# Kernel tuning notes

Hardware: AMD Instinct MI355X
Metric: run time of the kernel (lower is better)

The kernel has to match this reference:

```python
import jax, jax.numpy as jnp
import numpy as np

B, S, V = 2, 336, 8      # batch, seq_len, n_vars
D, H, P = 256, 8, 96     # d_model, num_heads, pred_len
DK = D // H
OUT_CHN = 8
EPS = 1e-5


def _layernorm(x, g, b):
    mu = jnp.mean(x, axis=-1, keepdims=True)
    var = jnp.var(x, axis=-1, keepdims=True)
    return (x - mu) * jax.lax.rsqrt(var + EPS) * g + b


def _attn_ff(src, Wq, bq, Wk, bk, Wv, bv, Wo, bo, ln1_g, ln1_b):
    # src: [N, L, D]; manual MHA + residual + layernorm (dropout=0)
    N, L, _ = src.shape
    q = (src @ Wq + bq).reshape(N, L, H, DK).transpose(0, 2, 1, 3)
    k = (src @ Wk + bk).reshape(N, L, H, DK).transpose(0, 2, 1, 3)
    v = (src @ Wv + bv).reshape(N, L, H, DK).transpose(0, 2, 1, 3)
    scores = jnp.einsum('nhqd,nhkd->nhqk', q, k) / np.sqrt(DK).astype(np.float32)
    attn = jax.nn.softmax(scores, axis=-1)
    o = jnp.einsum('nhqk,nhkd->nhqd', attn, v)
    o = o.transpose(0, 2, 1, 3).reshape(N, L, D) @ Wo + bo
    return _layernorm(src + o, ln1_g, ln1_b)


def setup_inputs() -> dict:
    key = jax.random.key(0)
    ks = jax.random.split(key, 8)
    s = 1.0 / np.sqrt(D)
    return {
        'x': jax.random.normal(ks[0], (B, S, V), dtype=jnp.float32),
        'emb_w': jax.random.normal(ks[1], (1, D), dtype=jnp.float32),
        'emb_b': jnp.zeros((D,), jnp.float32),
        'Wq': jax.random.normal(ks[2], (D, D), dtype=jnp.float32) * s,
        'bq': jnp.zeros((D,), jnp.float32),
        'Wk': jax.random.normal(ks[3], (D, D), dtype=jnp.float32) * s,
        'bk': jnp.zeros((D,), jnp.float32),
        'Wv': jax.random.normal(ks[4], (D, D), dtype=jnp.float32) * s,
        'bv': jnp.zeros((D,), jnp.float32),
        'Wo': jax.random.normal(ks[5], (D, D), dtype=jnp.float32) * s,
        'bo': jnp.zeros((D,), jnp.float32),
        'ln1_g': jnp.ones((D,), jnp.float32),
        'ln1_b': jnp.zeros((D,), jnp.float32),
        'norm_g': jnp.ones((D,), jnp.float32),
        'norm_b': jnp.zeros((D,), jnp.float32),
        'proj_w': jax.random.normal(ks[6], (S * D, P), dtype=jnp.float32) / np.sqrt(S * D).astype(np.float32),
        'proj_b': jnp.zeros((P,), jnp.float32),
    }


def reference(x, emb_w, emb_b, Wq, bq, Wk, bk, Wv, bv, Wo, bo,
              ln1_g, ln1_b, norm_g, norm_b, proj_w, proj_b):
    attn_p = (Wq, bq, Wk, bk, Wv, bv, Wo, bo, ln1_g, ln1_b)
    # x: [B,S,V] -> [B,V,S] -> embed each scalar to D
    e = x.transpose(0, 2, 1)[..., None] @ emb_w + emb_b  # [B,V,S,D]
    for _ in range(10):
        # attention over time axis (shared weights)
        e = _attn_ff(e.reshape(B * V, S, D), *attn_p).reshape(B, V, S, D)
        e = _layernorm(e.transpose(0, 2, 1, 3), norm_g, norm_b)  # [B,S,V,D]
        # attention over variable axis (same weights)
        e = _attn_ff(e.reshape(B * S, V, D), *attn_p).reshape(B, S, V, D)
        e = e.transpose(0, 2, 1, 3)  # [B,V,S,D]
    out = e.reshape(B, V, S * D) @ proj_w + proj_b  # [B,V,P]
    return out.transpose(0, 2, 1)[:, :, :OUT_CHN]  # [B,P,out_chn]
```

## Files before the change

### kernel.cpp

```cpp
#include <hip/hip_runtime.h>

#define SS 336
#define VV 8
#define DD 256
#define DKK 32
#define NTOK 5376
#define NTD (NTOK * DD)
#define ATT_SCALE 0.17677669529663687f
#define LN_EPS 1e-5f

typedef _Float16 f16x8 __attribute__((ext_vector_type(8)));
typedef _Float16 f16x4v __attribute__((ext_vector_type(4)));
typedef __attribute__((ext_vector_type(4))) float f32x4;

__device__ inline _Float16 f2h(float f) { return (_Float16)f; }

__global__ __launch_bounds__(256) void k_init(
    const float* __restrict__ Wq, const float* __restrict__ Wk,
    const float* __restrict__ Wv, const float* __restrict__ Wo,
    const float* __restrict__ x, const float* __restrict__ ew,
    const float* __restrict__ eb, const float* __restrict__ PB,
    const float* __restrict__ PW,
    _Float16* __restrict__ WT2, float* __restrict__ E,
    _Float16* __restrict__ E16, _Float16* __restrict__ PWF,
    float* __restrict__ out) {
  int bid = blockIdx.x;
  int tid = threadIdx.x;
  if (bid < 1024) {
    int z = bid >> 8;
    const float* W = (z == 0) ? Wq : (z == 1) ? Wk : (z == 2) ? Wv : Wo;
    int o = (bid & 255) * 256 + tid;
    int blk = o >> 9;
    int idx = o & 511;
    int lane = idx >> 3, j = idx & 7;
    int nt = blk >> 3, kb = blk & 7;
    int lcol = lane & 15, quad = lane >> 4;
    int n = nt * 16 + lcol;
    int k = kb * 32 + quad * 8 + j;
    WT2[(size_t)z * 65536 + o] = f2h(W[k * 256 + n]);
    if (bid == 0) {
      for (int i = tid; i < 1536; i += 256) {
        int row = i / 96, p = i - row * 96;
        out[(row >> 3) * 768 + p * 8 + (row & 7)] = PB[p];
      }
    }
  } else if (bid < 6400) {
    int token = bid - 1024;
    int n = token / SS, s = token - n * SS;
    int b = n >> 3, v = n & 7;
    float xv = x[(b * SS + s) * VV + v];
    int d = tid;
    float val = fmaf(xv, ew[d], eb[d]);
    E[token * DD + d] = val;
    E16[token * DD + d] = f2h(val);
  } else {
    int idx = (bid - 6400) * 256 + tid;
    int ktile = idx / 384;
    int rem = idx - ktile * 384;
    int nt = rem >> 6, lane = rem & 63;
    int quad = lane >> 4, lcol = lane & 15;
    int k0 = ktile * 32 + quad * 8;
    int n = nt * 16 + lcol;
    f16x8 w;
#pragma unroll
    for (int j = 0; j < 8; ++j) w[j] = f2h(PW[(size_t)(k0 + j) * 96 + n]);
    *(f16x8*)&PWF[(size_t)idx * 8] = w;
  }
}

#define KSTR 36
#define VTSTR 344
#define PSTR 72
#define QSTR 40
__global__ __launch_bounds__(512) void k_attn_time(
    const _Float16* __restrict__ Et16, const _Float16* __restrict__ Q16,
    const _Float16* __restrict__ K16, const _Float16* __restrict__ V16,
    const _Float16* __restrict__ WT2,
    const float* __restrict__ bq, const float* __restrict__ bk,
    const float* __restrict__ bv, _Float16* __restrict__ O16, int mode) {
  int qg = blockIdx.x, h = blockIdx.y, n = blockIdx.z;
  int tid = threadIdx.x;
  int wave = tid >> 6, lane = tid & 63;
  int quad = lane >> 4, lcol = lane & 15;

  __shared__ __align__(16) char SMRAW[143264];
  _Float16* Ks  = (_Float16*)SMRAW;
  _Float16* Vt  = (_Float16*)(SMRAW + 24192);
  _Float16* Qs  = (_Float16*)(SMRAW + 46240);
  _Float16* Wl  = (_Float16*)(SMRAW + 60320);
  _Float16* Ach = (_Float16*)(SMRAW + 109472);
  _Float16* PsB = (_Float16*)(mode ? SMRAW + 60320 : SMRAW + 46240);

  const size_t ebase = (size_t)(n * SS) * DD;
  const size_t base  = ebase + h * DKK;
  int qt0 = qg ? 11 : 0;
  int qtend = qg ? 21 : 11;

  const f32x4 z4 = {0.f, 0.f, 0.f, 0.f};

  if (mode) {
    {
      int h2 = h * 2;
      for (int c = tid; c < 3072; c += 512) {
        int ot = c >> 9, rest = c & 511;
        int z = (ot < 2) ? 1 : (ot < 4) ? 2 : 0;
        int nt = h2 + (ot & 1);
        *(f16x8*)&Wl[(ot << 12) + rest * 8] =
            *(const f16x8*)&WT2[(size_t)z * 65536 + nt * 4096 + rest * 8];
      }
      for (int c = tid; c < 272; c += 512) {
        if (c < 256) {
          int d = c >> 3, col = 336 + (c & 7);
          Vt[d * VTSTR + col] = (_Float16)0.f;
        } else {
          Vt[32 * VTSTR + (c - 256)] = (_Float16)0.f;
        }
      }
    }
    for (int ck = 0; ck < 6; ++ck) {
      int m0c = ck * 64;
      int nmt = (ck < 5) ? 4 : 1;
      __syncthreads();
      for (int c = tid; c < nmt * 16 * 32; c += 512) {
        int row = c >> 5, seg = c & 31;
        *(f16x8*)&Ach[row * 264 + seg * 8] =
            *(const f16x8*)&Et16[ebase + (size_t)(m0c + row) * 256 + seg * 8];
      }
      __syncthreads();
      int nU = nmt * 6;
      for (int u = wave; u < nU; u += 8) {
        int mtl = u / 6, ot = u % 6;
        int gt = ck * 4 + mtl;
        if (ot >= 4 && (gt < qt0 || gt >= qtend)) continue;
        f32x4 acc = z4;
#pragma unroll
        for (int kb = 0; kb < 8; ++kb) {
          f16x8 af = *(const f16x8*)&Ach[(mtl * 16 + lcol) * 264 + kb * 32 + quad * 8];
          f16x8 wf = *(const f16x8*)&Wl[(ot << 12) + kb * 512 + lane * 8];
          acc = __builtin_amdgcn_mfma_f32_16x16x32_f16(af, wf, acc, 0, 0, 0);
        }
        int dlo = ((ot & 1) << 4) + lcol;
        const float* bz = (ot < 2) ? bk : (ot < 4) ? bv : bq;
        float bval = bz[h * 32 + dlo];
        if (ot < 2) {
#pragma unroll
          for (int i = 0; i < 4; ++i)
            Ks[(m0c + mtl * 16 + quad * 4 + i) * KSTR + dlo] = f2h(acc[i] + bval);
        } else if (ot < 4) {
#pragma unroll
          for (int i = 0; i < 4; ++i)
            Vt[dlo * VTSTR + (m0c + mtl * 16 + quad * 4 + i)] = f2h(acc[i] + bval);
        } else {
          int ql = gt - qt0;
#pragma unroll
          for (int i = 0; i < 4; ++i)
            Qs[(ql * 16 + quad * 4 + i) * QSTR + dlo] = f2h(acc[i] + bval);
        }
      }
    }
    __syncthreads();
  } else {
    for (int c = tid; c < 1344; c += 512) {
      int row = c >> 2, part = c & 3;
      f16x8 kv = *(const f16x8*)&K16[base + (size_t)row * DD + part * 8];
      f16x4v klo = __builtin_shufflevector(kv, kv, 0, 1, 2, 3);
      f16x4v khi = __builtin_shufflevector(kv, kv, 4, 5, 6, 7);
      *(f16x4v*)&Ks[row * KSTR + part * 8] = klo;
      *(f16x4v*)&Ks[row * KSTR + part * 8 + 4] = khi;
      f16x8 vv = *(const f16x8*)&V16[base + (size_t)row * DD + part * 8];
#pragma unroll
      for (int j = 0; j < 8; ++j) Vt[(part * 8 + j) * VTSTR + row] = vv[j];
    }
    for (int c = tid; c < 272; c += 512) {
      if (c < 256) {
        int d = c >> 3, col = 336 + (c & 7);
        Vt[d * VTSTR + col] = (_Float16)0.f;
      } else {
        Vt[32 * VTSTR + (c - 256)] = (_Float16)0.f;
      }
    }
    __syncthreads();
  }

  _Float16* P = PsB + wave * (16 * PSTR);
  const f16x8 onesv = {(_Float16)1.f, (_Float16)1.f, (_Float16)1.f, (_Float16)1.f,
                       (_Float16)1.f, (_Float16)1.f, (_Float16)1.f, (_Float16)1.f};

  for (int qtile = qt0 + wave; qtile < qtend; qtile += 8) {
    int qb = qtile * 16;
    int ql = qtile - qt0;

    f16x8 qf;
    if (mode)
      qf = *(const f16x8*)&Qs[(ql * 16 + lcol) * QSTR + quad * 8];
    else
      qf = *(const f16x8*)&Q16[base + (size_t)(qb + lcol) * DD + quad * 8];
    f32x4 accA = {0.f, 0.f, 0.f, 0.f};
    f32x4 accB = {0.f, 0.f, 0.f, 0.f};
    f32x4 lacc = {0.f, 0.f, 0.f, 0.f};
    float m_[4] = {-1e30f, -1e30f, -1e30f, -1e30f};

    for (int T = 0; T < 6; ++T) {
      int k0 = T * 64;
      bool full = (T < 5);
      f32x4 s[4];
      {
        const _Float16* kp = &Ks[(k0 + lcol) * KSTR + quad * 8];
        f16x4v a0 = *(const f16x4v*)kp;
        f16x4v b0 = *(const f16x4v*)(kp + 4);
        f16x8 kf = __builtin_shufflevector(a0, b0, 0, 1, 2, 3, 4, 5, 6, 7);
        s[0] = __builtin_amdgcn_mfma_f32_16x16x32_f16(qf, kf, z4, 0, 0, 0);
      }
      if (full) {
#pragma unroll
        for (int u = 1; u < 4; ++u) {
          const _Float16* kp = &Ks[(k0 + u * 16 + lcol) * KSTR + quad * 8];
          f16x4v a0 = *(const f16x4v*)kp;
          f16x4v b0 = *(const f16x4v*)(kp + 4);
          f16x8 kf = __builtin_shufflevector(a0, b0, 0, 1, 2, 3, 4, 5, 6, 7);
          s[u] = __builtin_amdgcn_mfma_f32_16x16x32_f16(qf, kf, z4, 0, 0, 0);
        }
      } else {
        s[1] = z4; s[2] = z4; s[3] = z4;
      }
      float sc[4][4], p[4][4], corr[4];
#pragma unroll
      for (int u = 0; u < 4; ++u)
#pragma unroll
        for (int i = 0; i < 4; ++i)
          sc[u][i] = (u == 0 || full) ? s[u][i] * ATT_SCALE : -1e30f;
#pragma unroll
      for (int i = 0; i < 4; ++i) {
        float t2 = fmaxf(fmaxf(sc[0][i], sc[1][i]), fmaxf(sc[2][i], sc[3][i]));
        t2 = fmaxf(t2, __shfl_xor(t2, 1));
        t2 = fmaxf(t2, __shfl_xor(t2, 2));
        t2 = fmaxf(t2, __shfl_xor(t2, 4));
        t2 = fmaxf(t2, __shfl_xor(t2, 8));
        float nm = fmaxf(m_[i], t2);
        corr[i] = __expf(m_[i] - nm);
        m_[i] = nm;
#pragma unroll
        for (int u = 0; u < 4; ++u) p[u][i] = __expf(sc[u][i] - nm);
        accA[i] *= corr[i];
        accB[i] *= corr[i];
        lacc[i] *= corr[i];
      }
#pragma unroll
      for (int i = 0; i < 4; ++i)
#pragma unroll
        for (int u = 0; u < 4; ++u)
          P[(quad * 4 + i) * PSTR + u * 16 + lcol] = f2h(p[u][i]);
      f16x8 pf0 = *(const f16x8*)&P[lcol * PSTR + quad * 8];
      lacc = __builtin_amdgcn_mfma_f32_16x16x32_f16(pf0, onesv, lacc, 0, 0, 0);
      f16x8 va0 = *(const f16x8*)&Vt[lcol * VTSTR + k0 + quad * 8];
      f16x8 vb0 = *(const f16x8*)&Vt[(16 + lcol) * VTSTR + k0 + quad * 8];
      accA = __builtin_amdgcn_mfma_f32_16x16x32_f16(pf0, va0, accA, 0, 0, 0);
      accB = __builtin_amdgcn_mfma_f32_16x16x32_f16(pf0, vb0, accB, 0, 0, 0);
      if (full) {
        f16x8 pf1 = *(const f16x8*)&P[lcol * PSTR + 32 + quad * 8];
        lacc = __builtin_amdgcn_mfma_f32_16x16x32_f16(pf1, onesv, lacc, 0, 0, 0);
        f16x8 va1 = *(const f16x8*)&Vt[lcol * VTSTR + k0 + 32 + quad * 8];
        f16x8 vb1 = *(const f16x8*)&Vt[(16 + lcol) * VTSTR + k0 + 32 + quad * 8];
        accA = __builtin_amdgcn_mfma_f32_16x16x32_f16(pf1, va1, accA, 0, 0, 0);
        accB = __builtin_amdgcn_mfma_f32_16x16x32_f16(pf1, vb1, accB, 0, 0, 0);
      }
    }

#pragma unroll
    for (int i = 0; i < 4; ++i) {
      float inv = 1.f / lacc[i];
      P[(quad * 4 + i) * PSTR + lcol] = f2h(accA[i] * inv);
      P[(quad * 4 + i) * PSTR + 16 + lcol] = f2h(accB[i] * inv);
    }
    int row = lane >> 2, seg = lane & 3;
    f16x8 ov = *(const f16x8*)&P[row * PSTR + seg * 8];
    *(f16x8*)&O16[base + (size_t)(qb + row) * DD + seg * 8] = ov;
  }
}

__global__ __launch_bounds__(512) void k_mega_var(
    const _Float16* __restrict__ AO16, const _Float16* __restrict__ WT2,
    const float* __restrict__ bq, const float* __restrict__ bk,
    const float* __restrict__ bv, const float* __restrict__ bo,
    const float* __restrict__ g1, const float* __restrict__ c1,
    const float* __restrict__ gn, const float* __restrict__ bn,
    float* __restrict__ Etime, _Float16* __restrict__ Q16,
    _Float16* __restrict__ K16, _Float16* __restrict__ V16,
    _Float16* __restrict__ Et16, int doqkv) {
  int tid = threadIdx.x;
  int wave = tid >> 6, lane = tid & 63;
  int quad = lane >> 4, lcol = lane & 15;

  __shared__ int rmapS[32];
  __shared__ _Float16 Af[32 * 264];
  __shared__ float Cf[32 * 260];
  __shared__ _Float16 QKVs[32 * 776];

  if (tid < 32) {
    int r2 = blockIdx.x * 32 + tid;
    int n_idx = r2 >> 3, v = r2 & 7;
    int b = n_idx / SS, s = n_idx - b * SS;
    rmapS[tid] = (b * VV + v) * SS + s;
  }
  __syncthreads();

  {
    int row = tid >> 4, seg = tid & 15;
    const _Float16* src = AO16 + (size_t)rmapS[row] * DD + seg * 16;
    _Float16* dst = Af + row * 264 + seg * 16;
    *(f16x8*)(dst) = *(const f16x8*)(src);
    *(f16x8*)(dst + 8) = *(const f16x8*)(src + 8);
  }
  __syncthreads();

  const _Float16* WoF = WT2 + (size_t)3 * 65536;

  {
    f32x4 acc[2][2] = {};
    for (int kb = 0; kb < 8; ++kb) {
      int k0 = kb * 32;
      f16x8 af0 = *(const f16x8*)&Af[lcol * 264 + k0 + quad * 8];
      f16x8 af1 = *(const f16x8*)&Af[(16 + lcol) * 264 + k0 + quad * 8];
#pragma unroll
      for (int nt = 0; nt < 2; ++nt) {
        f16x8 bfr = *(const f16x8*)&WoF[((wave * 2 + nt) * 8 + kb) * 512 + lane * 8];
        acc[0][nt] = __builtin_amdgcn_mfma_f32_16x16x32_f16(af0, bfr, acc[0][nt], 0, 0, 0);
        acc[1][nt] = __builtin_amdgcn_mfma_f32_16x16x32_f16(af1, bfr, acc[1][nt], 0, 0, 0);
      }
    }
#pragma unroll
    for (int mt = 0; mt < 2; ++mt) {
#pragma unroll
      for (int i = 0; i < 4; ++i) {
        int row = mt * 16 + quad * 4 + i;
        size_t rb = (size_t)rmapS[row] * 256;
#pragma unroll
        for (int nt = 0; nt < 2; ++nt) {
          int col = (wave * 2 + nt) * 16 + lcol;
          Cf[row * 260 + col] = acc[mt][nt][i] + bo[col] + Etime[rb + col];
        }
      }
    }
  }
  __syncthreads();

  {
    int row = tid >> 4, c0 = (tid & 15) * 16;
    float v[16];
#pragma unroll
    for (int j = 0; j < 16; ++j) v[j] = Cf[row * 260 + c0 + j];
#pragma unroll
    for (int pass = 0; pass < 2; ++pass) {
      const float* gg = pass ? gn : g1;
      const float* bb = pass ? bn : c1;
      float s = 0.f, q = 0.f;
#pragma unroll
      for (int j = 0; j < 16; ++j) { s += v[j]; q = fmaf(v[j], v[j], q); }
      s += __shfl_xor(s, 1); q += __shfl_xor(q, 1);
      s += __shfl_xor(s, 2); q += __shfl_xor(q, 2);
      s += __shfl_xor(s, 4); q += __shfl_xor(q, 4);
      s += __shfl_xor(s, 8); q += __shfl_xor(q, 8);
      float mu = s * (1.0f / 256.0f);
      float rs = rsqrtf(q * (1.0f / 256.0f) - mu * mu + LN_EPS);
#pragma unroll
      for (int j = 0; j < 16; ++j)
        v[j] = fmaf((v[j] - mu) * rs, gg[c0 + j], bb[c0 + j]);
    }
#pragma unroll
    for (int j = 0; j < 16; ++j) Cf[row * 260 + c0 + j] = v[j];
#pragma unroll
    for (int j8 = 0; j8 < 2; ++j8) {
      f16x8 h;
#pragma unroll
      for (int jj = 0; jj < 8; ++jj) h[jj] = f2h(v[j8 * 8 + jj]);
      *(f16x8*)&Af[row * 264 + c0 + j8 * 8] = h;
    }
  }
  __syncthreads();

  {
    f32x4 acc[2][6] = {};
    for (int kb = 0; kb < 8; ++kb) {
      int k0 = kb * 32;
      f16x8 af0 = *(const f16x8*)&Af[lcol * 264 + k0 + quad * 8];
      f16x8 af1 = *(const f16x8*)&Af[(16 + lcol) * 264 + k0 + quad * 8];
#pragma unroll
      for (int j = 0; j < 6; ++j) {
        int ntg = wave * 6 + j;
        f16x8 bfr = *(const f16x8*)&WT2[(size_t)(ntg * 8 + kb) * 512 + lane * 8];
        acc[0][j] = __builtin_amdgcn_mfma_f32_16x16x32_f16(af0, bfr, acc[0][j], 0, 0, 0);
        acc[1][j] = __builtin_amdgcn_mfma_f32_16x16x32_f16(af1, bfr, acc[1][j], 0, 0, 0);
      }
    }
#pragma unroll
    for (int j = 0; j < 6; ++j) {
      int ntg = wave * 6 + j;
      int colb = ntg * 16;
      int z = colb >> 8, coln = (colb & 255) + lcol;
      const float* bz = (z == 0) ? bq : (z == 1) ? bk : bv;
      float bval = bz[coln];
#pragma unroll
      for (int mt = 0; mt < 2; ++mt) {
#pragma unroll
        for (int i = 0; i < 4; ++i)
          QKVs[(mt * 16 + quad * 4 + i) * 776 + colb + lcol] = f2h(acc[mt][j][i] + bval);
      }
    }
  }
  __syncthreads();

  {
    int half = tid & 1, qi = (tid >> 1) & 7, h = (tid >> 4) & 7, ng = tid >> 7;
    int d0 = h * 32 + half * 16;
    const _Float16* Qp = &QKVs[(ng * 8 + qi) * 776 + d0];
    float qv[16];
#pragma unroll
    for (int j8 = 0; j8 < 2; ++j8) {
      f16x8 t = *(const f16x8*)(Qp + j8 * 8);
#pragma unroll
      for (int jj = 0; jj < 8; ++jj) qv[j8 * 8 + jj] = (float)t[jj];
    }
    float sc[8];
#pragma unroll
    for (int k = 0; k < 8; ++k) {
      const _Float16* Kp = &QKVs[(ng * 8 + k) * 776 + 256 + d0];
      float s = 0.f;
#pragma unroll
      for (int j8 = 0; j8 < 2; ++j8) {
        f16x8 t = *(const f16x8*)(Kp + j8 * 8);
#pragma unroll
        for (int jj = 0; jj < 8; ++jj) s = fmaf(qv[j8 * 8 + jj], (float)t[jj], s);
      }
      sc[k] = s;
    }
#pragma unroll
    for (int k = 0; k < 8; ++k)
      sc[k] = (sc[k] + __shfl_xor(sc[k], 1)) * ATT_SCALE;
    float mx = sc[0];
#pragma unroll
    for (int k = 1; k < 8; ++k) mx = fmaxf(mx, sc[k]);
    float ps = 0.f;
#pragma unroll
    for (int k = 0; k < 8; ++k) { sc[k] = __expf(sc[k] - mx); ps += sc[k]; }
    float inv = 1.f / ps;
    float ov[16];
#pragma unroll
    for (int j = 0; j < 16; ++j) ov[j] = 0.f;
#pragma unroll
    for (int k = 0; k < 8; ++k) {
      const _Float16* Vp = &QKVs[(ng * 8 + k) * 776 + 512 + d0];
      float p = sc[k];
#pragma unroll
      for (int j8 = 0; j8 < 2; ++j8) {
        f16x8 t = *(const f16x8*)(Vp + j8 * 8);
#pragma unroll
        for (int jj = 0; jj < 8; ++jj)
          ov[j8 * 8 + jj] = fmaf(p, (float)t[jj], ov[j8 * 8 + jj]);
      }
    }
    _Float16* Op = &Af[(ng * 8 + qi) * 264 + d0];
#pragma unroll
    for (int j8 = 0; j8 < 2; ++j8) {
      f16x8 hh;
#pragma unroll
      for (int jj = 0; jj < 8; ++jj) hh[jj] = f2h(ov[j8 * 8 + jj] * inv);
      *(f16x8*)(Op + j8 * 8) = hh;
    }
  }
  __syncthreads();

  {
    f32x4 acc[2][2] = {};
    for (int kb = 0; kb < 8; ++kb) {
      int k0 = kb * 32;
      f16x8 af0 = *(const f16x8*)&Af[lcol * 264 + k0 + quad * 8];
      f16x8 af1 = *(const f16x8*)&Af[(16 + lcol) * 264 + k0 + quad * 8];
#pragma unroll
      for (int nt = 0; nt < 2; ++nt) {
        f16x8 bfr = *(const f16x8*)&WoF[((wave * 2 + nt) * 8 + kb) * 512 + lane * 8];
        acc[0][nt] = __builtin_amdgcn_mfma_f32_16x16x32_f16(af0, bfr, acc[0][nt], 0, 0, 0);
        acc[1][nt] = __builtin_amdgcn_mfma_f32_16x16x32_f16(af1, bfr, acc[1][nt], 0, 0, 0);
      }
    }
#pragma unroll
    for (int mt = 0; mt < 2; ++mt) {
#pragma unroll
      for (int i = 0; i < 4; ++i) {
        int row = mt * 16 + quad * 4 + i;
#pragma unroll
        for (int nt = 0; nt < 2; ++nt) {
          int col = (wave * 2 + nt) * 16 + lcol;
          Cf[row * 260 + col] = acc[mt][nt][i] + bo[col] + Cf[row * 260 + col];
        }
      }
    }
  }
  __syncthreads();

  {
    int row = tid >> 4, c0 = (tid & 15) * 16;
    float v[16];
#pragma unroll
    for (int j = 0; j < 16; ++j) v[j] = Cf[row * 260 + c0 + j];
    float s = 0.f, q = 0.f;
#pragma unroll
    for (int j = 0; j < 16; ++j) { s += v[j]; q = fmaf(v[j], v[j], q); }
    s += __shfl_xor(s, 1); q += __shfl_xor(q, 1);
    s += __shfl_xor(s, 2); q += __shfl_xor(q, 2);
    s += __shfl_xor(s, 4); q += __shfl_xor(q, 4);
    s += __shfl_xor(s, 8); q += __shfl_xor(q, 8);
    float mu = s * (1.0f / 256.0f);
    float rs = rsqrtf(q * (1.0f / 256.0f) - mu * mu + LN_EPS);
#pragma unroll
    for (int j = 0; j < 16; ++j)
      v[j] = fmaf((v[j] - mu) * rs, g1[c0 + j], c1[c0 + j]);
    size_t rb = (size_t)rmapS[row] * 256 + c0;
#pragma unroll
    for (int j4 = 0; j4 < 4; ++j4) {
      float4 f4 = make_float4(v[j4 * 4], v[j4 * 4 + 1], v[j4 * 4 + 2], v[j4 * 4 + 3]);
      *(float4*)&Etime[rb + j4 * 4] = f4;
    }
#pragma unroll
    for (int j8 = 0; j8 < 2; ++j8) {
      f16x8 hh;
#pragma unroll
      for (int jj = 0; jj < 8; ++jj) hh[jj] = f2h(v[j8 * 8 + jj]);
      *(f16x8*)&Af[row * 264 + c0 + j8 * 8] = hh;
      if (!doqkv) *(f16x8*)&Et16[rb + j8 * 8] = hh;
    }
  }
  __syncthreads();

  if (doqkv) {
    f32x4 acc[2][6] = {};
    for (int kb = 0; kb < 8; ++kb) {
      int k0 = kb * 32;
      f16x8 af0 = *(const f16x8*)&Af[lcol * 264 + k0 + quad * 8];
      f16x8 af1 = *(const f16x8*)&Af[(16 + lcol) * 264 + k0 + quad * 8];
#pragma unroll
      for (int j = 0; j < 6; ++j) {
        int ntg = wave * 6 + j;
        f16x8 bfr = *(const f16x8*)&WT2[(size_t)(ntg * 8 + kb) * 512 + lane * 8];
        acc[0][j] = __builtin_amdgcn_mfma_f32_16x16x32_f16(af0, bfr, acc[0][j], 0, 0, 0);
        acc[1][j] = __builtin_amdgcn_mfma_f32_16x16x32_f16(af1, bfr, acc[1][j], 0, 0, 0);
      }
    }
#pragma unroll
    for (int j = 0; j < 6; ++j) {
      int ntg = wave * 6 + j;
      int colb = ntg * 16;
      int z = colb >> 8, coln = (colb & 255) + lcol;
      const float* bz = (z == 0) ? bq : (z == 1) ? bk : bv;
      _Float16* Hd = (z == 0) ? Q16 : (z == 1) ? K16 : V16;
      float bval = bz[coln];
#pragma unroll
      for (int mt = 0; mt < 2; ++mt) {
#pragma unroll
        for (int i = 0; i < 4; ++i) {
          int row = mt * 16 + quad * 4 + i;
          Hd[(size_t)rmapS[row] * 256 + coln] = f2h(acc[mt][j][i] + bval);
        }
      }
    }
  }
}

__global__ __launch_bounds__(512) void k_proj(
    const _Float16* __restrict__ Et16, const _Float16* __restrict__ PWF,
    float* __restrict__ out) {
  __shared__ _Float16 Ets[16 * 1032];
  int tid = threadIdx.x;
  int wave = tid >> 6, lane = tid & 63;
  int quad = lane >> 4, lcol = lane & 15;
  int kt0 = blockIdx.x * 32;
  size_t kc0 = (size_t)kt0 * 32;

  for (int i = tid; i < 2048; i += 512) {
    int r = i >> 7, seg = i & 127;
    *(f16x8*)&Ets[r * 1032 + seg * 8] =
        *(const f16x8*)&Et16[(size_t)r * 86016 + kc0 + seg * 8];
  }
  __syncthreads();

  if (wave < 6) {
    f32x4 acc = {0.f, 0.f, 0.f, 0.f};
    const _Float16* bsrc = PWF + ((size_t)kt0 * 6 + wave) * 512 + lane * 8;
#pragma unroll 8
    for (int kt = 0; kt < 32; ++kt) {
      f16x8 af = *(const f16x8*)&Ets[lcol * 1032 + kt * 32 + quad * 8];
      f16x8 bf = *(const f16x8*)&bsrc[(size_t)kt * 6 * 512];
      acc = __builtin_amdgcn_mfma_f32_16x16x32_f16(af, bf, acc, 0, 0, 0);
    }
    int col = wave * 16 + lcol;
#pragma unroll
    for (int i = 0; i < 4; ++i) {
      int r = quad * 4 + i;
      atomicAdd(&out[(r >> 3) * 768 + col * 8 + (r & 7)], acc[i]);
    }
  }
}

extern "C" void kernel_launch(void* const* d_in, const int* in_sizes, int n_in,
                              void* d_out, int out_size, void* d_ws,
                              size_t ws_size, hipStream_t stream) {
  const float* x     = (const float*)d_in[0];
  const float* emb_w = (const float*)d_in[1];
  const float* emb_b = (const float*)d_in[2];
  const float* Wq = (const float*)d_in[3];
  const float* bq = (const float*)d_in[4];
  const float* Wk = (const float*)d_in[5];
  const float* bk = (const float*)d_in[6];
  const float* Wv = (const float*)d_in[7];
  const float* bv = (const float*)d_in[8];
  const float* Wo = (const float*)d_in[9];
  const float* bo = (const float*)d_in[10];
  const float* g1 = (const float*)d_in[11];
  const float* b1 = (const float*)d_in[12];
  const float* gn = (const float*)d_in[13];
  const float* bn = (const float*)d_in[14];
  const float* PW = (const float*)d_in[15];
  const float* PB = (const float*)d_in[16];
  float* out = (float*)d_out;

  float* ws = (float*)d_ws;
  float* Etime   = ws;
  _Float16* Et16 = (_Float16*)(ws + (size_t)NTD);
  _Float16* Q16  = (_Float16*)(ws + (size_t)NTD + NTD / 2);
  _Float16* K16  = Q16 + (size_t)NTD;
  _Float16* V16  = K16 + (size_t)NTD;
  _Float16* AO16 = V16 + (size_t)NTD;
  _Float16* WT2  = AO16 + (size_t)NTD;
  _Float16* PWF  = WT2 + 4 * 65536;

  k_init<<<10432, 256, 0, stream>>>(Wq, Wk, Wv, Wo, x, emb_w, emb_b, PB, PW,
                                    WT2, Etime, Et16, PWF, out);
  for (int it = 0; it < 10; ++it) {
    k_attn_time<<<dim3(2, 8, 16), 512, 0, stream>>>(
        Et16, Q16, K16, V16, WT2, bq, bk, bv, AO16, (it == 0) ? 1 : 0);
    k_mega_var<<<168, 512, 0, stream>>>(
        AO16, WT2, bq, bk, bv, bo, g1, b1, gn, bn, Etime,
        Q16, K16, V16, Et16, (it < 9) ? 1 : 0);
  }
  k_proj<<<84, 512, 0, stream>>>(Et16, PWF, out);
}
```

Baseline: 555.1 us.

## Fuse final projection into last variable-attention kernel and pad V-transpose stride

The separate projection kernel is removed. On the final iteration, k_mega_var now multiplies its normalized fp16 rows in shared memory directly by the pre-packed projection weights and atomically adds into the output. This avoids the extra launch and the write and re-read of the fp16 activations. The transposed-V shared-memory stride also grows from 344 to 348 to change the bank mapping, with a larger pad to zero and slightly more LDS.

New measurement: 600.5 us. 8.2% more time.

```diff
diff --git a/kernel.cpp b/kernel.cpp
--- a/kernel.cpp
+++ b/kernel.cpp
@@ -69,7 +69,7 @@
 }
 
 #define KSTR 36
-#define VTSTR 344
+#define VTSTR 348
 #define PSTR 72
 #define QSTR 40
 __global__ __launch_bounds__(512) void k_attn_time(
@@ -83,13 +83,13 @@
   int wave = tid >> 6, lane = tid & 63;
   int quad = lane >> 4, lcol = lane & 15;
 
-  __shared__ __align__(16) char SMRAW[143264];
+  __shared__ __align__(16) char SMRAW[143520];
   _Float16* Ks  = (_Float16*)SMRAW;
   _Float16* Vt  = (_Float16*)(SMRAW + 24192);
-  _Float16* Qs  = (_Float16*)(SMRAW + 46240);
-  _Float16* Wl  = (_Float16*)(SMRAW + 60320);
-  _Float16* Ach = (_Float16*)(SMRAW + 109472);
-  _Float16* PsB = (_Float16*)(mode ? SMRAW + 60320 : SMRAW + 46240);
+  _Float16* Qs  = (_Float16*)(SMRAW + 46496);
+  _Float16* Wl  = (_Float16*)(SMRAW + 60576);
+  _Float16* Ach = (_Float16*)(SMRAW + 109728);
+  _Float16* PsB = (_Float16*)(mode ? SMRAW + 60576 : SMRAW + 46496);
 
   const size_t ebase = (size_t)(n * SS) * DD;
   const size_t base  = ebase + h * DKK;
@@ -108,12 +108,12 @@
         *(f16x8*)&Wl[(ot << 12) + rest * 8] =
             *(const f16x8*)&WT2[(size_t)z * 65536 + nt * 4096 + rest * 8];
       }
-      for (int c = tid; c < 272; c += 512) {
-        if (c < 256) {
-          int d = c >> 3, col = 336 + (c & 7);
+      for (int c = tid; c < 400; c += 512) {
+        if (c < 384) {
+          int d = c / 12, col = 336 + (c % 12);
           Vt[d * VTSTR + col] = (_Float16)0.f;
         } else {
-          Vt[32 * VTSTR + (c - 256)] = (_Float16)0.f;
+          Vt[32 * VTSTR + (c - 384)] = (_Float16)0.f;
         }
       }
     }
@@ -171,12 +171,12 @@
 #pragma unroll
       for (int j = 0; j < 8; ++j) Vt[(part * 8 + j) * VTSTR + row] = vv[j];
     }
-    for (int c = tid; c < 272; c += 512) {
-      if (c < 256) {
-        int d = c >> 3, col = 336 + (c & 7);
+    for (int c = tid; c < 400; c += 512) {
+      if (c < 384) {
+        int d = c / 12, col = 336 + (c % 12);
         Vt[d * VTSTR + col] = (_Float16)0.f;
       } else {
-        Vt[32 * VTSTR + (c - 256)] = (_Float16)0.f;
+        Vt[32 * VTSTR + (c - 384)] = (_Float16)0.f;
       }
     }
     __syncthreads();
@@ -280,13 +280,14 @@
 
 __global__ __launch_bounds__(512) void k_mega_var(
     const _Float16* __restrict__ AO16, const _Float16* __restrict__ WT2,
+    const _Float16* __restrict__ PWF,
     const float* __restrict__ bq, const float* __restrict__ bk,
     const float* __restrict__ bv, const float* __restrict__ bo,
     const float* __restrict__ g1, const float* __restrict__ c1,
     const float* __restrict__ gn, const float* __restrict__ bn,
     float* __restrict__ Etime, _Float16* __restrict__ Q16,
     _Float16* __restrict__ K16, _Float16* __restrict__ V16,
-    _Float16* __restrict__ Et16, int doqkv) {
+    float* __restrict__ out, int doqkv) {
   int tid = threadIdx.x;
   int wave = tid >> 6, lane = tid & 63;
   int quad = lane >> 4, lcol = lane & 15;
@@ -526,7 +527,6 @@
 #pragma unroll
       for (int jj = 0; jj < 8; ++jj) hh[jj] = f2h(v[j8 * 8 + jj]);
       *(f16x8*)&Af[row * 264 + c0 + j8 * 8] = hh;
-      if (!doqkv) *(f16x8*)&Et16[rb + j8 * 8] = hh;
     }
   }
   __syncthreads();
@@ -562,40 +562,30 @@
         }
       }
     }
-  }
-}
-
-__global__ __launch_bounds__(512) void k_proj(
-    const _Float16* __restrict__ Et16, const _Float16* __restrict__ PWF,
-    float* __restrict__ out) {
-  __shared__ _Float16 Ets[16 * 1032];
-  int tid = threadIdx.x;
-  int wave = tid >> 6, lane = tid & 63;
-  int quad = lane >> 4, lcol = lane & 15;
-  int kt0 = blockIdx.x * 32;
-  size_t kc0 = (size_t)kt0 * 32;
-
-  for (int i = tid; i < 2048; i += 512) {
-    int r = i >> 7, seg = i & 127;
-    *(f16x8*)&Ets[r * 1032 + seg * 8] =
-        *(const f16x8*)&Et16[(size_t)r * 86016 + kc0 + seg * 8];
-  }
-  __syncthreads();
-
-  if (wave < 6) {
-    f32x4 acc = {0.f, 0.f, 0.f, 0.f};
-    const _Float16* bsrc = PWF + ((size_t)kt0 * 6 + wave) * 512 + lane * 8;
-#pragma unroll 8
-    for (int kt = 0; kt < 32; ++kt) {
-      f16x8 af = *(const f16x8*)&Ets[lcol * 1032 + kt * 32 + quad * 8];
-      f16x8 bf = *(const f16x8*)&bsrc[(size_t)kt * 6 * 512];
-      acc = __builtin_amdgcn_mfma_f32_16x16x32_f16(af, bf, acc, 0, 0, 0);
-    }
-    int col = wave * 16 + lcol;
-#pragma unroll
-    for (int i = 0; i < 4; ++i) {
-      int r = quad * 4 + i;
-      atomicAdd(&out[(r >> 3) * 768 + col * 8 + (r & 7)], acc[i]);
+  } else {
+    if (wave < 6) {
+      int nt = wave;
+      int b_ = (blockIdx.x >= 84) ? 1 : 0;
+      int s0 = blockIdx.x * 4 - b_ * SS;
+      f32x4 acc = {0.f, 0.f, 0.f, 0.f};
+#pragma unroll
+      for (int sg = 0; sg < 4; ++sg) {
+        int s = s0 + sg;
+#pragma unroll
+        for (int kb = 0; kb < 8; ++kb) {
+          f16x8 af = *(const f16x8*)&Af[(sg * 8 + (lcol & 7)) * 264 + kb * 32 + quad * 8];
+          f16x8 bf = *(const f16x8*)&PWF[(((size_t)(s * 8 + kb)) * 6 + nt) * 512 + lane * 8];
+          acc = __builtin_amdgcn_mfma_f32_16x16x32_f16(af, bf, acc, 0, 0, 0);
+        }
+      }
+      if (quad < 2) {
+        int p = nt * 16 + lcol;
+#pragma unroll
+        for (int i = 0; i < 4; ++i) {
+          int v = quad * 4 + i;
+          atomicAdd(&out[b_ * 768 + p * 8 + v], acc[i]);
+        }
+      }
     }
   }
 }
@@ -638,8 +628,7 @@
     k_attn_time<<<dim3(2, 8, 16), 512, 0, stream>>>(
         Et16, Q16, K16, V16, WT2, bq, bk, bv, AO16, (it == 0) ? 1 : 0);
     k_mega_var<<<168, 512, 0, stream>>>(
-        AO16, WT2, bq, bk, bv, bo, g1, b1, gn, bn, Etime,
-        Q16, K16, V16, Et16, (it < 9) ? 1 : 0);
-  }
-  k_proj<<<84, 512, 0, stream>>>(Et16, PWF, out);
+        AO16, WT2, PWF, bq, bk, bv, bo, g1, b1, gn, bn, Etime,
+        Q16, K16, V16, out, (it < 9) ? 1 : 0);
+  }
 }
```
